# Kernel tuning notes

Measured on AMD Instinct MI355X. Metric: run time of the kernel, lower is better.

The kernel has to match this reference:

```python
import jax, jax.numpy as jnp
import numpy as np

RADIUS = 4
SIGMA_I = 10.0
SIGMA_X = 4.0
NUM_CLASSES = 8
PAD = RADIUS - 1          # 3, ConstantPad3d(radius-1, eps)
WIN = 2 * PAD + 1         # 7x7x7 window
EPS = float(np.finfo(np.float64).eps)


def _dist_flat():
    # spatial gaussian, zero outside the ball x^2+y^2+z^2 < radius^2
    r = np.arange(1 - RADIUS, RADIUS)
    xx, yy, zz = np.meshgrid(r, r, r, indexing='ij')
    d2 = (xx ** 2 + yy ** 2 + zz ** 2).astype(np.float32)
    dist = np.where(d2 < RADIUS ** 2, np.exp(-d2 / SIGMA_X ** 2), 0.0).astype(np.float32)
    return jnp.asarray(dist.reshape(-1))  # flattened x-major, matches i = x*49 + y*7 + z


def setup_inputs() -> dict:
    key = jax.random.key(0)
    k1, k2 = jax.random.split(key)
    batch = jax.random.normal(k1, (4, 1, 32, 32, 32), dtype=jnp.float32)
    preds = jax.random.uniform(k2, (4, 8, 32, 32, 32), dtype=jnp.float32)
    return {"batch": batch, "preds": preds}


def reference(batch, preds):
    B, _, D, H, W = batch.shape
    K = preds.shape[1]
    pad_cfg = ((0, 0), (0, 0), (PAD, PAD), (PAD, PAD), (PAD, PAD))
    pb = jnp.pad(batch, pad_cfg, constant_values=EPS)
    pp = jnp.pad(preds, pad_cfg, constant_values=EPS)
    dist_flat = _dist_flat()
    inv_sI2 = jnp.float32(1.0 / (SIGMA_I ** 2))

    def step(carry, i):
        numer, sumw = carry
        x = i // (WIN * WIN)
        y = (i // WIN) % WIN
        z = i % WIN
        sb = jax.lax.dynamic_slice(pb, (0, 0, x, y, z), (B, 1, D, H, W))
        sp = jax.lax.dynamic_slice(pp, (0, 0, x, y, z), (B, K, D, H, W))
        # affinity = intensity gaussian * spatial gaussian for this offset
        aff = jnp.exp(-jnp.square(batch - sb) * inv_sI2) * dist_flat[i]
        return (numer + aff * sp, sumw + aff), None

    init = (jnp.zeros((B, K, D, H, W), batch.dtype),
            jnp.zeros((B, 1, D, H, W), batch.dtype))
    (numer, sumw), _ = jax.lax.scan(step, init, jnp.arange(WIN ** 3))

    assocA = jnp.sum(numer * preds, axis=(2, 3, 4))  # (B, K)
    assocV = jnp.sum(sumw * preds, axis=(2, 3, 4))   # (B, K)
    return NUM_CLASSES - jnp.sum(assocA / assocV, axis=-1)  # (B,)
```

## Files before the change

kernel.cpp:

```cpp
#include <hip/hip_runtime.h>
#include <hip/hip_fp16.h>


#define EPS_F 2.220446049250313e-16f

constexpr int TD = 4, TH = 8, TW = 8;
constexpr int HDh = 7, HHh = 14, HWh = 14;
constexpr int SYB = 17;
constexpr int SXB = HHh * SYB;
constexpr int NB  = 6 * SXB + 13 * SYB + 13 + 1;
constexpr int NT = 512;
constexpr int NBLK = 512;
constexpr int NTASK = HDh * HHh * 4;

#define K1F (-0.014426950408889634f)
#define K2F (-0.09016844005556021f)

struct Ent { int off; float lw; };
struct Tab { Ent e[64]; int n; };

constexpr Tab make_tab(int half) {
    Tab t{};
    t.n = 0;
    for (int dxq = 0; dxq < 4; ++dxq)
        for (int dyi = 0; dyi < 7; ++dyi)
            for (int dzi = 0; dzi < 7; ++dzi) {
                int dy = dyi - 3, dz = dzi - 3;
                if (dxq == 0) {
                    if (dy < 0) continue;
                    if (dy == 0 && dz <= 0) continue;
                }
                int c2 = dxq * dxq + dy * dy + dz * dz;
                if (c2 >= 16) continue;
                if (((dyi + dzi) & 1) != half) continue;
                t.e[t.n].off = dxq * SXB + dy * SYB + dz;
                t.e[t.n].lw  = (float)c2 * K2F;
                ++t.n;
            }
    return t;
}
constexpr Tab TAB0 = make_tab(0);
constexpr Tab TAB1 = make_tab(1);

constexpr float W16[16] = {
    1.0f,                    0.93941306281347578611f, 0.88249690258459546286f,
    0.82902911818040034301f, 0.77880078307140486825f, 0.73161562894664190813f,
    0.68728927879097219970f, 0.64565423513106973593f, 0.60653065971263342360f,
    0.56978282473092302544f, 0.53526142851899028012f, 0.50283157797094090696f,
    0.47236655274101470713f, 0.44374731008100323837f, 0.41686201967850837523f,
    0.39160740400665634335f };

struct STab { float s[343]; };
constexpr STab make_stab() {
    STab t{};
    for (int a = 0; a < 7; ++a)
        for (int b = 0; b < 7; ++b)
            for (int c = 0; c < 7; ++c) {
                const int pa = a < 3 ? a : (a == 3 ? 16 : a + 25);
                const int pb = b < 3 ? b : (b == 3 ? 16 : b + 25);
                const int pc = c < 3 ? c : (c == 3 ? 16 : c + 25);
                float s = 0.f;
                for (int dx = -3; dx <= 3; ++dx)
                    for (int dy = -3; dy <= 3; ++dy)
                        for (int dz = -3; dz <= 3; ++dz) {
                            const int c2 = dx * dx + dy * dy + dz * dz;
                            if (c2 >= 16) continue;
                            const bool neg = (dx < 0) ||
                                (dx == 0 && (dy < 0 || (dy == 0 && dz < 0)));
                            if (!neg) continue;
                            const bool in = (pa + dx) >= 0 && (pa + dx) < 32 &&
                                            (pb + dy) >= 0 && (pb + dy) < 32 &&
                                            (pc + dz) >= 0 && (pc + dz) < 32;
                            if (!in) s += W16[c2];
                        }
                t.s[(a * 7 + b) * 7 + c] = s;
            }
    return t;
}
__constant__ STab STAB = make_stab();

__device__ __forceinline__ int bcls(int p) {
    return p < 3 ? p : (p > 28 ? p - 25 : 3);
}

__device__ __forceinline__ unsigned pack2(float a, float b) {
    return (unsigned)__half_as_ushort(__float2half(a)) |
           ((unsigned)__half_as_ushort(__float2half(b)) << 16);
}

template <int HALF>
__device__ __forceinline__ void accum_pairs(const float* __restrict__ sB,
                                            const uint4* __restrict__ sPk,
                                            int vown, float b_own,
                                            float acc[9]) {
    constexpr Tab T = HALF ? TAB1 : TAB0;
    constexpr int N = HALF ? TAB1.n : TAB0.n;
    constexpr int N4 = (N / 4) * 4;

#pragma unroll
    for (int i = 0; i < N4; i += 4) {
        float sb[4];
        uint4 pk[4];
#pragma unroll
        for (int j = 0; j < 4; ++j) {
            const int nv = vown + T.e[i + j].off;
            sb[j] = sB[nv];
            pk[j] = sPk[nv];
        }
#pragma unroll
        for (int j = 0; j < 4; ++j) {
            const float d = b_own - sb[j];
            const float aff =
                __builtin_amdgcn_exp2f(__builtin_fmaf(d * d, K1F, T.e[i + j].lw));
            acc[8] += aff;
            __half2 h[4];
            __builtin_memcpy(h, &pk[j], 16);
            acc[0] = __builtin_fmaf(aff, __half2float(__low2half(h[0])),  acc[0]);
            acc[1] = __builtin_fmaf(aff, __half2float(__high2half(h[0])), acc[1]);
            acc[2] = __builtin_fmaf(aff, __half2float(__low2half(h[1])),  acc[2]);
            acc[3] = __builtin_fmaf(aff, __half2float(__high2half(h[1])), acc[3]);
            acc[4] = __builtin_fmaf(aff, __half2float(__low2half(h[2])),  acc[4]);
            acc[5] = __builtin_fmaf(aff, __half2float(__high2half(h[2])), acc[5]);
            acc[6] = __builtin_fmaf(aff, __half2float(__low2half(h[3])),  acc[6]);
            acc[7] = __builtin_fmaf(aff, __half2float(__high2half(h[3])), acc[7]);
        }
    }
#pragma unroll
    for (int i = N4; i < N; ++i) {
        const int nv = vown + T.e[i].off;
        const float sb = sB[nv];
        const uint4 pk = sPk[nv];
        const float d = b_own - sb;
        const float aff =
            __builtin_amdgcn_exp2f(__builtin_fmaf(d * d, K1F, T.e[i].lw));
        acc[8] += aff;
        __half2 h[4];
        __builtin_memcpy(h, &pk, 16);
        acc[0] = __builtin_fmaf(aff, __half2float(__low2half(h[0])),  acc[0]);
        acc[1] = __builtin_fmaf(aff, __half2float(__high2half(h[0])), acc[1]);
        acc[2] = __builtin_fmaf(aff, __half2float(__low2half(h[1])),  acc[2]);
        acc[3] = __builtin_fmaf(aff, __half2float(__high2half(h[1])), acc[3]);
        acc[4] = __builtin_fmaf(aff, __half2float(__low2half(h[2])),  acc[4]);
        acc[5] = __builtin_fmaf(aff, __half2float(__high2half(h[2])), acc[5]);
        acc[6] = __builtin_fmaf(aff, __half2float(__low2half(h[3])),  acc[6]);
        acc[7] = __builtin_fmaf(aff, __half2float(__high2half(h[3])), acc[7]);
    }
}

__global__ __launch_bounds__(NT, 4)
void softncuts_main(const float* __restrict__ batch,
                    const float* __restrict__ preds,
                    float* __restrict__ partials) {
    __shared__ float sB[NB];
    __shared__ uint4 sPk[NB];
    __shared__ float valsT[NT * 20];

    const int bid  = blockIdx.x;
    const int bb   = bid >> 7;
    const int tile = bid & 127;
    const int tw = tile & 3;
    const int th = (tile >> 2) & 3;
    const int td = tile >> 4;
    const int d0 = td * TD, h0 = th * TH, w0 = tw * TW;

    const int tid  = threadIdx.x;
    const int half = tid >> 8;
    const int vtid = tid & 255;
    const int lw = vtid & 7;
    const int lh = (vtid >> 3) & 7;
    const int ld = vtid >> 6;

    const float* bbase = batch + (size_t)bb * 32768;
    const float* pbase = preds + (size_t)bb * 8 * 32768;

    if (tid < NTASK) {
        const int t   = tid;
        const int c   = t & 3;
        const int row = t >> 2;
        const int hh  = row % HHh;
        const int hd  = row / HHh;
        const int gd  = d0 + hd;
        const int gh  = h0 + hh - 3;
        const int gw0 = w0 - 4 + c * 4;
        const int hwb = c * 4 - 1;
        const bool fast = (gd < 32) & ((unsigned)gh < 32u) & (gw0 >= 0) & (gw0 + 3 < 32);
        if (fast) {
            const int sidx = (gd * 32 + gh) * 32 + gw0;
            float4 pv[9];
            pv[0] = *(const float4*)(bbase + sidx);
#pragma unroll
            for (int k = 0; k < 8; ++k)
                pv[k + 1] = *(const float4*)(pbase + sidx + k * 32768);
#pragma unroll
            for (int e = 0; e < 4; ++e) {
                const int hw = hwb + e;
                if (hw < 0 || hw >= HWh) continue;
                const int f = hd * SXB + hh * SYB + hw;
                sB[f] = ((const float*)&pv[0])[e];
                unsigned u[4];
#pragma unroll
                for (int k = 0; k < 4; ++k)
                    u[k] = pack2(((const float*)&pv[2 * k + 1])[e],
                                 ((const float*)&pv[2 * k + 2])[e]);
                sPk[f] = make_uint4(u[0], u[1], u[2], u[3]);
            }
        } else {
#pragma unroll
            for (int e = 0; e < 4; ++e) {
                const int hw = hwb + e;
                if (hw < 0 || hw >= HWh) continue;
                const int gw = gw0 + e;
                const bool in = (gd < 32) & ((unsigned)gh < 32u) & ((unsigned)gw < 32u);
                const int sidx = (gd * 32 + gh) * 32 + gw;
                const int f = hd * SXB + hh * SYB + hw;
                sB[f] = in ? bbase[sidx] : EPS_F;
                unsigned u[4];
#pragma unroll
                for (int k = 0; k < 4; ++k)
                    u[k] = pack2(in ? pbase[sidx + (2 * k) * 32768]     : 0.f,
                                 in ? pbase[sidx + (2 * k + 1) * 32768] : 0.f);
                sPk[f] = make_uint4(u[0], u[1], u[2], u[3]);
            }
        }
    }
    __syncthreads();

    const int gdo = d0 + ld, gho = h0 + lh, gwo = w0 + lw;
    const int sidx_own = (gdo * 32 + gho) * 32 + gwo;
    const float b_own = bbase[sidx_own];
    float q[8];
#pragma unroll
    for (int k = 0; k < 8; ++k) q[k] = pbase[sidx_own + k * 32768];

    const int vown = ld * SXB + (lh + 3) * SYB + (lw + 3);

    float acc[9];
#pragma unroll
    for (int i = 0; i < 9; ++i) acc[i] = 0.f;

    if (half == 0) accum_pairs<0>(sB, sPk, vown, b_own, acc);
    else           accum_pairs<1>(sB, sPk, vown, b_own, acc);

    float selfpad = 0.f;
    if (half == 0) {
        const float S = STAB.s[(bcls(gdo) * 7 + bcls(gho)) * 7 + bcls(gwo)];
        const float db = b_own - EPS_F;
        selfpad = 1.f + S * __expf(db * db * -0.01f);
    }

    float vals[16];
#pragma unroll
    for (int k = 0; k < 8; ++k) {
        vals[k]     = q[k] * (2.f * acc[k] + ((half == 0) ? q[k] : 0.f));
        vals[8 + k] = q[k] * (acc[8] + selfpad) + acc[k];
    }

    {
        float* vr = &valsT[tid * 20];
        ((float4*)vr)[0] = make_float4(vals[0],  vals[1],  vals[2],  vals[3]);
        ((float4*)vr)[1] = make_float4(vals[4],  vals[5],  vals[6],  vals[7]);
        ((float4*)vr)[2] = make_float4(vals[8],  vals[9],  vals[10], vals[11]);
        ((float4*)vr)[3] = make_float4(vals[12], vals[13], vals[14], vals[15]);
    }
    __syncthreads();
    {
        const int val = tid >> 5;
        const int r   = tid & 31;
        float s = 0.f;
#pragma unroll
        for (int k = 0; k < 16; ++k)
            s += valsT[(r + 32 * k) * 20 + val];
        for (int off = 16; off; off >>= 1) s += __shfl_down(s, off, 32);
        if (r == 0) partials[val * NBLK + bid] = s;
    }
}

__global__ __launch_bounds__(1024)
void softncuts_finalize(const float* __restrict__ partials,
                        float* __restrict__ out) {
    __shared__ float red[64];
    const int tid = threadIdx.x;
    const int group = tid >> 4;
    const int j0 = tid & 15;
    const int slot = group & 15;
    const int bb = group >> 4;

    const float* p = partials + slot * NBLK + bb * 128;
    float s = 0.f;
#pragma unroll
    for (int k = 0; k < 8; ++k) s += p[j0 + 16 * k];
    for (int off = 8; off; off >>= 1) s += __shfl_down(s, off, 16);
    if (j0 == 0) red[group] = s;
    __syncthreads();

    if (tid < 4) {
        float accv = 0.f;
#pragma unroll
        for (int k = 0; k < 8; ++k)
            accv += red[tid * 16 + k] / red[tid * 16 + 8 + k];
        out[tid] = 8.0f - accv;
    }
}

extern "C" void kernel_launch(void* const* d_in, const int* in_sizes, int n_in,
                              void* d_out, int out_size, void* d_ws, size_t ws_size,
                              hipStream_t stream) {
    const float* batch = (const float*)d_in[0];
    const float* preds = (const float*)d_in[1];
    float* out      = (float*)d_out;
    float* partials = (float*)d_ws;

    softncuts_main<<<dim3(NBLK), dim3(NT), 0, stream>>>(batch, preds, partials);
    softncuts_finalize<<<dim3(1), dim3(1024), 0, stream>>>(partials, out);
}
```

Baseline: 78.48 us.

## Split neighbor offsets four ways across 1024-thread blocks with aliased shared memory

Each block now runs 1024 threads, with four thread groups per output voxel instead of two. Each group handles a quarter of the half-space neighbor offsets, assigned round-robin from the offset table. The staging buffers and the reduction buffer now share one LDS allocation, so LDS per block stays about the same despite twice the threads. The block reduction becomes a two-phase fold: the upper 512 threads write first and the lower 512 add their values in. This raises parallelism per tile but adds extra barriers and cuts registers per thread under launch_bounds(1024, 8).

```diff
diff --git a/kernel.cpp b/kernel.cpp
--- a/kernel.cpp
+++ b/kernel.cpp
@@ -9,19 +9,21 @@
 constexpr int SYB = 17;
 constexpr int SXB = HHh * SYB;
 constexpr int NB  = 6 * SXB + 13 * SYB + 13 + 1;
-constexpr int NT = 512;
+constexpr int NT = 1024;
 constexpr int NBLK = 512;
 constexpr int NTASK = HDh * HHh * 4;
 
+constexpr int SB_BYTES  = ((NB * 4 + 15) / 16) * 16;
+constexpr int LDS_BYTES = 512 * 20 * 4;
+
 #define K1F (-0.014426950408889634f)
 #define K2F (-0.09016844005556021f)
 
 struct Ent { int off; float lw; };
-struct Tab { Ent e[64]; int n; };
-
-constexpr Tab make_tab(int half) {
-    Tab t{};
-    t.n = 0;
+struct QTab { Ent e[32]; int n; };
+
+constexpr QTab make_qtab(int cls) {
+    QTab t{}; t.n = 0; int idx = 0;
     for (int dxq = 0; dxq < 4; ++dxq)
         for (int dyi = 0; dyi < 7; ++dyi)
             for (int dzi = 0; dzi < 7; ++dzi) {
@@ -32,15 +34,18 @@
                 }
                 int c2 = dxq * dxq + dy * dy + dz * dz;
                 if (c2 >= 16) continue;
-                if (((dyi + dzi) & 1) != half) continue;
+                const int my = idx & 3; ++idx;
+                if (my != cls) continue;
                 t.e[t.n].off = dxq * SXB + dy * SYB + dz;
                 t.e[t.n].lw  = (float)c2 * K2F;
                 ++t.n;
             }
     return t;
 }
-constexpr Tab TAB0 = make_tab(0);
-constexpr Tab TAB1 = make_tab(1);
+constexpr QTab QT0 = make_qtab(0);
+constexpr QTab QT1 = make_qtab(1);
+constexpr QTab QT2 = make_qtab(2);
+constexpr QTab QT3 = make_qtab(3);
 
 constexpr float W16[16] = {
     1.0f,                    0.93941306281347578611f, 0.88249690258459546286f,
@@ -88,13 +93,13 @@
            ((unsigned)__half_as_ushort(__float2half(b)) << 16);
 }
 
-template <int HALF>
-__device__ __forceinline__ void accum_pairs(const float* __restrict__ sB,
-                                            const uint4* __restrict__ sPk,
-                                            int vown, float b_own,
-                                            float acc[9]) {
-    constexpr Tab T = HALF ? TAB1 : TAB0;
-    constexpr int N = HALF ? TAB1.n : TAB0.n;
+template <int CLS>
+__device__ __forceinline__ void accum_q(const float* __restrict__ sB,
+                                        const uint4* __restrict__ sPk,
+                                        int vown, float b_own,
+                                        float acc[9]) {
+    constexpr QTab T = CLS == 0 ? QT0 : CLS == 1 ? QT1 : CLS == 2 ? QT2 : QT3;
+    constexpr int N = T.n;
     constexpr int N4 = (N / 4) * 4;
 
 #pragma unroll
@@ -147,13 +152,14 @@
     }
 }
 
-__global__ __launch_bounds__(NT, 4)
+__global__ __launch_bounds__(NT, 8)
 void softncuts_main(const float* __restrict__ batch,
                     const float* __restrict__ preds,
                     float* __restrict__ partials) {
-    __shared__ float sB[NB];
-    __shared__ uint4 sPk[NB];
-    __shared__ float valsT[NT * 20];
+    __shared__ __align__(16) unsigned char smem[LDS_BYTES];
+    float* const sB    = (float*)smem;
+    uint4* const sPk   = (uint4*)(smem + SB_BYTES);
+    float* const valsT = (float*)smem;
 
     const int bid  = blockIdx.x;
     const int bb   = bid >> 7;
@@ -164,11 +170,6 @@
     const int d0 = td * TD, h0 = th * TH, w0 = tw * TW;
 
     const int tid  = threadIdx.x;
-    const int half = tid >> 8;
-    const int vtid = tid & 255;
-    const int lw = vtid & 7;
-    const int lh = (vtid >> 3) & 7;
-    const int ld = vtid >> 6;
 
     const float* bbase = batch + (size_t)bb * 32768;
     const float* pbase = preds + (size_t)bb * 8 * 32768;
@@ -225,24 +226,35 @@
     }
     __syncthreads();
 
+    const int cid  = tid >> 8;
+    const int vtid = tid & 255;
+    const int lw = vtid & 7;
+    const int lh = (vtid >> 3) & 7;
+    const int ld = vtid >> 6;
+
     const int gdo = d0 + ld, gho = h0 + lh, gwo = w0 + lw;
     const int sidx_own = (gdo * 32 + gho) * 32 + gwo;
     const float b_own = bbase[sidx_own];
+
+    const int vown = ld * SXB + (lh + 3) * SYB + (lw + 3);
+
+    float acc[9];
+#pragma unroll
+    for (int i = 0; i < 9; ++i) acc[i] = 0.f;
+
+    switch (cid) {
+        case 0:  accum_q<0>(sB, sPk, vown, b_own, acc); break;
+        case 1:  accum_q<1>(sB, sPk, vown, b_own, acc); break;
+        case 2:  accum_q<2>(sB, sPk, vown, b_own, acc); break;
+        default: accum_q<3>(sB, sPk, vown, b_own, acc); break;
+    }
+
     float q[8];
 #pragma unroll
     for (int k = 0; k < 8; ++k) q[k] = pbase[sidx_own + k * 32768];
 
-    const int vown = ld * SXB + (lh + 3) * SYB + (lw + 3);
-
-    float acc[9];
-#pragma unroll
-    for (int i = 0; i < 9; ++i) acc[i] = 0.f;
-
-    if (half == 0) accum_pairs<0>(sB, sPk, vown, b_own, acc);
-    else           accum_pairs<1>(sB, sPk, vown, b_own, acc);
-
     float selfpad = 0.f;
-    if (half == 0) {
+    if (cid == 0) {
         const float S = STAB.s[(bcls(gdo) * 7 + bcls(gho)) * 7 + bcls(gwo)];
         const float db = b_own - EPS_F;
         selfpad = 1.f + S * __expf(db * db * -0.01f);
@@ -251,19 +263,34 @@
     float vals[16];
 #pragma unroll
     for (int k = 0; k < 8; ++k) {
-        vals[k]     = q[k] * (2.f * acc[k] + ((half == 0) ? q[k] : 0.f));
+        vals[k]     = q[k] * (2.f * acc[k] + ((cid == 0) ? q[k] : 0.f));
         vals[8 + k] = q[k] * (acc[8] + selfpad) + acc[k];
     }
 
-    {
-        float* vr = &valsT[tid * 20];
+    __syncthreads();
+    if (tid >= 512) {
+        float* vr = &valsT[(tid - 512) * 20];
         ((float4*)vr)[0] = make_float4(vals[0],  vals[1],  vals[2],  vals[3]);
         ((float4*)vr)[1] = make_float4(vals[4],  vals[5],  vals[6],  vals[7]);
         ((float4*)vr)[2] = make_float4(vals[8],  vals[9],  vals[10], vals[11]);
         ((float4*)vr)[3] = make_float4(vals[12], vals[13], vals[14], vals[15]);
     }
     __syncthreads();
-    {
+    if (tid < 512) {
+        float* vr = &valsT[tid * 20];
+        float4 p0 = ((float4*)vr)[0], p1 = ((float4*)vr)[1];
+        float4 p2 = ((float4*)vr)[2], p3 = ((float4*)vr)[3];
+        ((float4*)vr)[0] = make_float4(vals[0]  + p0.x, vals[1]  + p0.y,
+                                       vals[2]  + p0.z, vals[3]  + p0.w);
+        ((float4*)vr)[1] = make_float4(vals[4]  + p1.x, vals[5]  + p1.y,
+                                       vals[6]  + p1.z, vals[7]  + p1.w);
+        ((float4*)vr)[2] = make_float4(vals[8]  + p2.x, vals[9]  + p2.y,
+                                       vals[10] + p2.z, vals[11] + p2.w);
+        ((float4*)vr)[3] = make_float4(vals[12] + p3.x, vals[13] + p3.y,
+                                       vals[14] + p3.z, vals[15] + p3.w);
+    }
+    __syncthreads();
+    if (tid < 512) {
         const int val = tid >> 5;
         const int r   = tid & 31;
         float s = 0.f;
```

After: 78.73 us. No clear change (+0.3%).
